# Kernel tuning notes

Measured on AMD Instinct MI355X. Metric: run time of the kernel, lower is better.

## Reference

```python
import jax, jax.numpy as jnp
import numpy as np

BS, P, D, C, ND, K, NC, H = 32, 196, 512, 100, 51, 50, 800, 8
LAMBDA, BETA, EPS = 0.5, 5.5, 1e-5


def _ln(x, g, b):
    m = x.mean(-1, keepdims=True)
    v = jnp.mean((x - m) ** 2, axis=-1, keepdims=True)
    return (x - m) / jnp.sqrt(v + EPS) * g + b


def _norm(x):
    return x / jnp.linalg.norm(x, axis=-1, keepdims=True)


def _bonder(x, kv, Wq, Wk, Wv, Wo, ln1_g, ln1_b, ln2_g, ln2_b, W1, b1, W2, b2):
    # cross-attn block: queries = text prompts [B,N,d], kv = retrieved patch feats [B,M,d]
    B, N, d = x.shape
    M = kv.shape[1]
    dh = d // H
    q = (_ln(x, ln1_g, ln1_b) @ Wq).reshape(B, N, H, dh)
    k = (kv @ Wk).reshape(B, M, H, dh)
    v = (kv @ Wv).reshape(B, M, H, dh)
    att = jax.nn.softmax(jnp.einsum('bnhd,bmhd->bhnm', q, k) / np.sqrt(dh).astype(np.float32), axis=-1)
    o = jnp.einsum('bhnm,bmhd->bnhd', att, v).reshape(B, N, d) @ Wo
    x = x + o
    h = _ln(x, ln2_g, ln2_b)
    return x + jax.nn.gelu(h @ W1 + b1) @ W2 + b2


def _dense_logits(gfeat, local, all_text, mean_text, topk):
    # gfeat [b,d], local [b,p,d], all_text [C,n,d], mean_text [C,d]
    base = gfeat @ mean_text.T                                   # [b,C]
    w = jnp.einsum('bd,bpd->bp', gfeat, local)                   # [b,p]
    atf = jnp.transpose(all_text, (1, 0, 2))                     # [n,C,d]
    v = jax.nn.softmax(jnp.einsum('cd,ncd->nc', mean_text, atf), axis=0)  # [n,C]
    sim = jnp.einsum('bpd,ncd->bcpn', local, atf)                # [b,C,p,n]
    vals, idx = jax.lax.top_k(jnp.transpose(sim, (0, 1, 3, 2)), topk)     # over patch dim
    sim_topk = jnp.transpose(vals, (0, 1, 3, 2))                 # [b,C,k,n]
    idx = jnp.transpose(idx, (0, 1, 3, 2))                       # [b,C,k,n]
    idx_w = idx[:, 0, :, 0]                                      # [b,k]
    w_topk = jax.nn.softmax(jnp.take_along_axis(w, idx_w, axis=1), axis=-1)  # [b,k]
    weight = jnp.einsum('bk,nc->bckn', w_topk, v)                # [b,C,k,n]
    return base + jnp.sum(sim_topk * weight, axis=(-2, -1))


def setup_inputs() -> dict:
    key = jax.random.key(0)
    ks = jax.random.split(key, 12)
    s = 0.02
    labels = jax.random.randint(ks[10], (BS,), 0, C)
    cache_labels = jax.random.randint(ks[11], (NC,), 0, C)
    return {
        'local_feat': jax.random.normal(ks[0], (BS, P, D)),
        'Wa': jnp.eye(D) + s * jax.random.normal(ks[1], (D, D)),
        'text_cache': jax.random.normal(ks[2], (C, ND, D)),
        'Wq': s * jax.random.normal(ks[3], (D, D)),
        'Wk': s * jax.random.normal(ks[4], (D, D)),
        'Wv': s * jax.random.normal(ks[5], (D, D)),
        'Wo': s * jax.random.normal(ks[6], (D, D)),
        'ln1_g': jnp.ones((D,)), 'ln1_b': jnp.zeros((D,)),
        'ln2_g': jnp.ones((D,)), 'ln2_b': jnp.zeros((D,)),
        'W1': s * jax.random.normal(ks[7], (D, 4 * D)), 'b1': jnp.zeros((4 * D,)),
        'W2': s * jax.random.normal(ks[8], (4 * D, D)), 'b2': jnp.zeros((D,)),
        'logit_scale': jnp.asarray(np.log(1.0 / 0.07), jnp.float32),
        'ensemble_scale': jnp.asarray(-2.0, jnp.float32),
        'raw_cache_local_feats': jax.random.normal(ks[9], (NC, P, D)),
        'cache_values': jax.nn.one_hot(cache_labels, C, dtype=jnp.float32),
        'labels': labels,
        'cache_labels': cache_labels,
    }


def reference(local_feat, Wa, text_cache, Wq, Wk, Wv, Wo, ln1_g, ln1_b, ln2_g, ln2_b,
              W1, b1, W2, b2, logit_scale, ensemble_scale, raw_cache_local_feats,
              cache_values, labels, cache_labels):
    bs = local_feat.shape[0]
    adapted_local = _norm(local_feat @ Wa.T)                      # [b,p,d]
    adapted_global = _norm(adapted_local.mean(axis=1))            # [b,d]
    base_text_mean = _norm(jax.lax.stop_gradient(text_cache).mean(axis=1))  # [C,d]
    sim_to_text = jax.lax.stop_gradient(adapted_local @ base_text_mean.T)   # [b,p,C]
    sim_target = sim_to_text[jnp.arange(bs), :, labels]           # [b,p]
    topk_idx = jax.lax.top_k(sim_target, K)[1]
    botk_idx = jax.lax.top_k(-sim_target, K)[1]
    topk_feats = jnp.take_along_axis(adapted_local, topk_idx[:, :, None], axis=1)  # [b,K,d]
    botk_feats = jnp.take_along_axis(adapted_local, botk_idx[:, :, None], axis=1)
    # training branch: bonder on ground-truth class prompts, scatter into bias_full
    l2p = text_cache[labels]                                      # [b,ND,d]
    text_bias = _bonder(l2p, jax.lax.stop_gradient(topk_feats),
                        Wq, Wk, Wv, Wo, ln1_g, ln1_b, ln2_g, ln2_b, W1, b1, W2, b2)
    bias_full = jnp.zeros((bs, C, ND, D), local_feat.dtype).at[jnp.arange(bs), labels].set(text_bias)
    bias_avg = bias_full.mean(axis=0)                             # [C,ND,d]
    refined = text_cache + LAMBDA * bias_avg
    refined_norm = _norm(refined)
    refined_mean_norm = _norm(refined_norm.mean(axis=1))
    ls = jnp.exp(logit_scale)
    inter = ls * _dense_logits(adapted_global, adapted_local, refined_norm, refined_mean_norm, K)
    # tip-adapter cache branch
    cache_adapted = _norm(raw_cache_local_feats @ Wa.T)           # [Nc,p,d]
    cache_sim = jax.lax.stop_gradient(cache_adapted @ base_text_mean.T)
    cache_sim_target = cache_sim[jnp.arange(cache_sim.shape[0]), :, cache_labels]
    cache_topk_idx = jax.lax.top_k(cache_sim_target, K)[1]
    cache_topk_feats = jnp.take_along_axis(cache_adapted, cache_topk_idx[:, :, None], axis=1)
    cache_keys = _norm(cache_topk_feats.mean(axis=1))             # [Nc,d]
    query_keys = _norm(topk_feats.mean(axis=1))                   # [b,d]
    affinity = jnp.exp(-BETA * (1.0 - query_keys @ cache_keys.T))
    intra = affinity @ cache_values                               # [b,C]
    scale = jax.nn.sigmoid(ensemble_scale)
    logits = inter * (1 - scale) + intra * ls * scale
    return (logits, inter, intra, adapted_global, topk_feats, botk_feats, refined_norm)
```

## Files before the change

kernel.cpp:

```cpp
#include <hip/hip_runtime.h>
#include <math.h>

#define DEV static __device__ __forceinline__

typedef __attribute__((ext_vector_type(8))) short short8v;
typedef __attribute__((ext_vector_type(8))) _Float16 half8v;
typedef __attribute__((ext_vector_type(4))) float f32x4;

DEV unsigned encf(float f){ unsigned b=__float_as_uint(f); return b ^ (0x80000000u | (unsigned)((int)b>>31)); }
DEV unsigned long long pkvi(float v, int idx){
  return ((unsigned long long)encf(v)<<32) | (unsigned long long)(0xffffffffu - (unsigned)idx);
}
DEV unsigned long long wave_max_ull(unsigned long long u){
  #pragma unroll
  for (int m=1;m<64;m<<=1){ unsigned long long o = __shfl_xor(u, m); if (o>u) u=o; }
  return u;
}
DEV float wave_sum(float v){
  #pragma unroll
  for (int m=32;m;m>>=1) v += __shfl_xor(v, m);
  return v;
}
DEV float blk_sum256(float v, float* scr){
  v = wave_sum(v);
  __syncthreads();
  if ((threadIdx.x & 63)==0) scr[threadIdx.x>>6] = v;
  __syncthreads();
  return scr[0]+scr[1]+scr[2]+scr[3];
}
DEV float gelu_f(float x){ return 0.5f*x*(1.f + tanhf(0.7978845608028654f*(x + 0.044715f*x*x*x))); }
DEV unsigned short f2bf(float x){
  unsigned u = __float_as_uint(x);
  unsigned r = (u + 0x7fffu + ((u>>16)&1u)) >> 16;
  return (unsigned short)r;
}
DEV float bf2f(unsigned short h){ return __uint_as_float(((unsigned)h)<<16); }
DEV void gld16(const void* g, void* l){
  __builtin_amdgcn_global_load_lds((const __attribute__((address_space(1))) unsigned int*)g,
                                   (__attribute__((address_space(3))) unsigned int*)l, 16, 0, 0);
}
template<int CTRL>
DEV float dppf(float x){
  return __int_as_float(__builtin_amdgcn_mov_dpp(__float_as_int(x), CTRL, 0xF, 0xF, false));
}

template<bool TRANSB, int EPI>
__global__ __launch_bounds__(256,2) void gemm128(
  const float* __restrict__ A, const float* __restrict__ B, float* __restrict__ Cp,
  const int M, const int N, const int K,
  const float* __restrict__ bias, const float* __restrict__ resid)
{
  __shared__ float As[16][132];
  __shared__ float Bs[16][132];
  const int t = threadIdx.x;
  const int row0 = blockIdx.x*128, col0 = blockIdx.y*128;
  const int tx = t & 15, ty = t >> 4;
  float acc[8][8];
  #pragma unroll
  for (int i=0;i<8;++i)
    #pragma unroll
    for (int j=0;j<8;++j) acc[i][j]=0.f;

  for (int k0=0; k0<K; k0+=16){
    #pragma unroll
    for (int it=0; it<2; ++it){
      int f = t + it*256;
      int m = f >> 2, kq = (f & 3) << 2;
      float4 v = make_float4(0.f,0.f,0.f,0.f);
      int gr = row0 + m;
      if (gr < M) v = *(const float4*)(A + (size_t)gr*K + (k0+kq));
      As[kq+0][m]=v.x; As[kq+1][m]=v.y; As[kq+2][m]=v.z; As[kq+3][m]=v.w;
    }
    if (TRANSB){
      #pragma unroll
      for (int it=0; it<2; ++it){
        int f = t + it*256;
        int n = f >> 2, kq = (f & 3) << 2;
        float4 v = make_float4(0.f,0.f,0.f,0.f);
        int gc = col0 + n;
        if (gc < N) v = *(const float4*)(B + (size_t)gc*K + (k0+kq));
        Bs[kq+0][n]=v.x; Bs[kq+1][n]=v.y; Bs[kq+2][n]=v.z; Bs[kq+3][n]=v.w;
      }
    } else {
      #pragma unroll
      for (int it=0; it<2; ++it){
        int f = t + it*256;
        int kk = f >> 5, n4 = (f & 31) << 2;
        float4 v = *(const float4*)(B + (size_t)(k0+kk)*N + (col0+n4));
        *(float4*)&Bs[kk][n4] = v;
      }
    }
    __syncthreads();
    #pragma unroll
    for (int k=0;k<16;++k){
      float a[8], bb[8];
      *(float4*)&a[0] = *(const float4*)&As[k][ty*4];
      *(float4*)&a[4] = *(const float4*)&As[k][64+ty*4];
      *(float4*)&bb[0] = *(const float4*)&Bs[k][tx*4];
      *(float4*)&bb[4] = *(const float4*)&Bs[k][64+tx*4];
      #pragma unroll
      for (int i=0;i<8;++i)
        #pragma unroll
        for (int j=0;j<8;++j) acc[i][j] = fmaf(a[i], bb[j], acc[i][j]);
    }
    __syncthreads();
  }

  #pragma unroll
  for (int i=0;i<8;++i){
    int gr = row0 + ((i<4)? (ty*4+i) : (64+ty*4+i-4));
    if (gr >= M) continue;
    #pragma unroll
    for (int jb=0;jb<2;++jb){
      int gc = col0 + (jb? (64+tx*4) : (tx*4));
      float4 vv;
      vv.x = acc[i][jb*4+0]; vv.y = acc[i][jb*4+1]; vv.z = acc[i][jb*4+2]; vv.w = acc[i][jb*4+3];
      if (EPI & 1){
        const float4 bv = *(const float4*)(bias + gc);
        vv.x += bv.x; vv.y += bv.y; vv.z += bv.z; vv.w += bv.w;
      }
      if (EPI & 2){
        vv.x = gelu_f(vv.x); vv.y = gelu_f(vv.y); vv.z = gelu_f(vv.z); vv.w = gelu_f(vv.w);
      }
      if (EPI & 4){
        const float4 rv = *(const float4*)(resid + (size_t)gr*N + gc);
        vv.x += rv.x; vv.y += rv.y; vv.z += rv.z; vv.w += rv.w;
      }
      *(float4*)(Cp + (size_t)gr*N + gc) = vv;
    }
  }
}

template<bool TRANS, bool SUBI>
__global__ __launch_bounds__(256) void k_convw(const float* __restrict__ W,
    unsigned short* __restrict__ hi, unsigned short* __restrict__ lo, int R, int C){
  int n = blockIdx.x;
  int K = TRANS ? R : C;
  for (int k = threadIdx.x; k < K; k += 256){
    float x = TRANS ? W[(size_t)k*C + n] : W[(size_t)n*C + k];
    if (SUBI && k==n) x -= 1.f;
    unsigned short h = f2bf(x);
    hi[(size_t)n*K + k] = h;
    if (lo) lo[(size_t)n*K + k] = f2bf(x - bf2f(h));
  }
}

__global__ __launch_bounds__(256) void k_convw4(
  const float* __restrict__ Wq, const float* __restrict__ Wk,
  const float* __restrict__ Wv, const float* __restrict__ Wo,
  unsigned short* __restrict__ qh, unsigned short* __restrict__ ql,
  unsigned short* __restrict__ kh, unsigned short* __restrict__ kl,
  unsigned short* __restrict__ vh, unsigned short* __restrict__ vl,
  unsigned short* __restrict__ oh, unsigned short* __restrict__ ol)
{
  int n = blockIdx.x;
  const float* W; unsigned short *hi, *lo;
  switch(blockIdx.y){
    case 0: W=Wq; hi=qh; lo=ql; break;
    case 1: W=Wk; hi=kh; lo=kl; break;
    case 2: W=Wv; hi=vh; lo=vl; break;
    default: W=Wo; hi=oh; lo=ol; break;
  }
  for (int k = threadIdx.x; k < 512; k += 256){
    float x = W[(size_t)k*512 + n];
    unsigned short h = f2bf(x);
    hi[(size_t)n*512 + k] = h;
    lo[(size_t)n*512 + k] = f2bf(x - bf2f(h));
  }
}

__global__ __launch_bounds__(256) void k_convd2(const float* __restrict__ Wa, unsigned short* __restrict__ Dfrag){
  int e = blockIdx.x;
  int tile = e>>4, lr = e&15;
  for (int d = threadIdx.x; d < 512; d += 256){
    float x = Wa[(size_t)e*512 + d] - (e==d ? 1.f : 0.f);
    union { _Float16 hh; unsigned short u; } cv;
    cv.hh = (_Float16)x;
    int ks = d>>5, q = (d>>3)&3, el = d&7;
    Dfrag[(size_t)(((tile*16+ks)*64 + q*16 + lr)*8 + el)] = cv.u;
  }
}

template<int EPI>
__global__ __launch_bounds__(256,2) void gemmAB(
  const unsigned short* __restrict__ Ahi, const unsigned short* __restrict__ Alo,
  const unsigned short* __restrict__ Bhi, const unsigned short* __restrict__ Blo,
  float* __restrict__ Cp, unsigned short* __restrict__ Chi, unsigned short* __restrict__ Clo,
  const int M, const int N, const int K,
  const float* __restrict__ bias, const float* __restrict__ resid)
{
  __shared__ __align__(16) char sm[32768];
  const int t = threadIdx.x, lane = t&63, wid = t>>6;
  const int row0 = blockIdx.x*128, col0 = blockIdx.y*128;
  f32x4 acc[2][8];
  #pragma unroll
  for (int i=0;i<2;++i)
    #pragma unroll
    for (int j=0;j<8;++j) acc[i][j] = (f32x4){0.f,0.f,0.f,0.f};

  int offA[2], offB[8];
  #pragma unroll
  for (int mt=0; mt<2; ++mt){
    int row = (2*wid+mt)*16 + (lane&15);
    int sp = (lane>>4) ^ ((row>>1)&3);
    offA[mt] = row*64 + sp*16;
  }
  #pragma unroll
  for (int nt=0; nt<8; ++nt){
    int row = nt*16 + (lane&15);
    int sp = (lane>>4) ^ ((row>>1)&3);
    offB[nt] = row*64 + sp*16;
  }

  const int nks = K >> 5;
  for (int ks=0; ks<nks; ++ks){
    #pragma unroll
    for (int i=0;i<2;++i){
      int s = i*256 + t, row = s>>2, sl2 = s&3, slog = sl2 ^ ((row>>1)&3);
      size_t ga = (size_t)(row0+row)*K + ks*32 + slog*8;
      size_t gb = (size_t)(col0+row)*K + ks*32 + slog*8;
      int dst = (i*256 + wid*64)*16;
      gld16(Ahi + ga, sm + dst);
      gld16(Alo + ga, sm + 8192 + dst);
      gld16(Bhi + gb, sm + 16384 + dst);
      gld16(Blo + gb, sm + 24576 + dst);
    }
    __syncthreads();
    short8v ah0 = *(short8v*)(sm + offA[0]);
    short8v ah1 = *(short8v*)(sm + offA[1]);
    short8v al0 = *(short8v*)(sm + 8192 + offA[0]);
    short8v al1 = *(short8v*)(sm + 8192 + offA[1]);
    #pragma unroll
    for (int nt=0; nt<8; ++nt){
      short8v bh = *(short8v*)(sm + 16384 + offB[nt]);
      short8v bl = *(short8v*)(sm + 24576 + offB[nt]);
      acc[0][nt] = __builtin_amdgcn_mfma_f32_16x16x32_bf16(ah0, bh, acc[0][nt], 0,0,0);
      acc[0][nt] = __builtin_amdgcn_mfma_f32_16x16x32_bf16(ah0, bl, acc[0][nt], 0,0,0);
      acc[0][nt] = __builtin_amdgcn_mfma_f32_16x16x32_bf16(al0, bh, acc[0][nt], 0,0,0);
      acc[1][nt] = __builtin_amdgcn_mfma_f32_16x16x32_bf16(ah1, bh, acc[1][nt], 0,0,0);
      acc[1][nt] = __builtin_amdgcn_mfma_f32_16x16x32_bf16(ah1, bl, acc[1][nt], 0,0,0);
      acc[1][nt] = __builtin_amdgcn_mfma_f32_16x16x32_bf16(al1, bh, acc[1][nt], 0,0,0);
    }
    __syncthreads();
  }

  #pragma unroll
  for (int mt=0; mt<2; ++mt){
    #pragma unroll
    for (int nt=0; nt<8; ++nt){
      int n = col0 + nt*16 + (lane&15);
      int mb = row0 + (2*wid+mt)*16 + (lane>>4)*4;
      #pragma unroll
      for (int j=0;j<4;++j){
        int m = mb + j;
        if (m < M){
          float v = acc[mt][nt][j];
          if (EPI & 1) v += bias[n];
          if (EPI & 2) v = gelu_f(v);
          if (EPI & 4) v += resid[(size_t)m*N + n];
          if (EPI & 8){
            unsigned short h = f2bf(v);
            Chi[(size_t)m*N + n] = h;
            Clo[(size_t)m*N + n] = f2bf(v - bf2f(h));
          } else {
            Cp[(size_t)m*N + n] = v;
          }
        }
      }
    }
  }
}

__global__ __launch_bounds__(256,2) void gemmABQKV(
  const unsigned short* __restrict__ lnH, const unsigned short* __restrict__ lnL,
  const unsigned short* __restrict__ tkH, const unsigned short* __restrict__ tkL,
  const unsigned short* __restrict__ qh, const unsigned short* __restrict__ ql,
  const unsigned short* __restrict__ kh, const unsigned short* __restrict__ kl,
  const unsigned short* __restrict__ vh, const unsigned short* __restrict__ vl,
  float* __restrict__ qb, float* __restrict__ kb, float* __restrict__ vbuf)
{
  __shared__ __align__(16) char sm[32768];
  const int z = blockIdx.z;
  const unsigned short* Ahi = (z==0)? lnH : tkH;
// ... 176 lines not shown
          float rh = (float)*(const _Float16*)(Alds + kse*8192 + row*64 + sll*16 + (o&7)*2);
          p = fmaf(U, 2.f*rh + U, p);
        }
        p += __shfl_xor(p,1); p += __shfl_xor(p,2); p += __shfl_xor(p,4); p += __shfl_xor(p,8);
        pacc[mt][j] += p;
      }
    }
  }

  __syncthreads();
  if ((lane&15)==0){
    #pragma unroll
    for (int mt=0; mt<4; ++mt)
      #pragma unroll
      for (int j=0;j<4;++j)
        n2x[wn][wm*64 + mt*16 + (lane>>4)*4 + j] = pacc[mt][j];
  }
  __syncthreads();
  if (t < 128)
    norm2[m0+t] = n2sq[t] + n2x[0][t] + n2x[1][t] + n2x[2][t] + n2x[3][t];
}

__global__ __launch_bounds__(256) void k_rownorm(const float* __restrict__ in, float* __restrict__ out,
                                                 unsigned short* __restrict__ bfo, int nrows){
  __shared__ float scr[4];
  int r = blockIdx.x, t = threadIdx.x; (void)nrows;
  const float* p = in + (size_t)r*512;
  float x0 = p[t], x1 = p[t+256];
  float ss = blk_sum256(x0*x0 + x1*x1, scr);
  float inv = 1.f/sqrtf(ss);
  float v0 = x0*inv, v1 = x1*inv;
  out[(size_t)r*512 + t] = v0;
  out[(size_t)r*512 + t + 256] = v1;
  if (bfo){
    size_t br = (size_t)(r/196)*256 + (r%196);
    bfo[br*512 + t]     = f2bf(v0);
    bfo[br*512 + t+256] = f2bf(v1);
  }
}

__global__ __launch_bounds__(256) void k_meanrows_norm(const float* __restrict__ in, int nper,
                                                       float* __restrict__ o1, float* __restrict__ o2){
  __shared__ float scr[4];
  int g = blockIdx.x, t = threadIdx.x;
  float s0=0.f, s1=0.f;
  const float* bp = in + (size_t)g*nper*512;
  for (int r=0;r<nper;++r){ s0 += bp[(size_t)r*512+t]; s1 += bp[(size_t)r*512+t+256]; }
  float ss = blk_sum256(s0*s0+s1*s1, scr);
  float inv = 1.f/sqrtf(ss);
  float v0 = s0*inv, v1 = s1*inv;
  o1[(size_t)g*512+t]=v0; o1[(size_t)g*512+t+256]=v1;
  if (o2){ o2[(size_t)g*512+t]=v0; o2[(size_t)g*512+t+256]=v1; }
}

__global__ __launch_bounds__(256) void k_zmat(const float* __restrict__ btm, const float* __restrict__ Wa, float* __restrict__ z){
  int c = blockIdx.x, t = threadIdx.x;
  float a0=0.f, a1=0.f;
  for (int d=0; d<512; ++d){
    float bv = btm[c*512+d];
    a0 = fmaf(bv, Wa[(size_t)d*512+t], a0);
    a1 = fmaf(bv, Wa[(size_t)d*512+t+256], a1);
  }
  z[c*512+t]=a0; z[c*512+t+256]=a1;
}

__global__ __launch_bounds__(256) void k_dot_bp(const float* __restrict__ AL, const float* __restrict__ vecs,
                                                const int* __restrict__ sel, float* __restrict__ outv, int mode){
  int wid = blockIdx.x*4 + (threadIdx.x>>6);
  int lane = threadIdx.x & 63;
  int b = wid/196;
  int vrow = sel ? sel[b] : (mode ? 0 : b);
  const float* a = AL + (size_t)wid*512 + lane*8;
  const float* v = vecs + (size_t)vrow*512 + lane*8;
  float4 a0 = *(const float4*)a, a1 = *(const float4*)(a+4);
  float4 v0 = *(const float4*)v, v1 = *(const float4*)(v+4);
  float s = a0.x*v0.x + a0.y*v0.y + a0.z*v0.z + a0.w*v0.w
          + a1.x*v1.x + a1.y*v1.y + a1.z*v1.z + a1.w*v1.w;
  s = wave_sum(s);
  if (lane==0) outv[wid] = s;
}

__global__ __launch_bounds__(256) void k_dot2(const float* __restrict__ AL, const float* __restrict__ AGw,
                                              const float* __restrict__ RN00,
                                              float* __restrict__ wbp, float* __restrict__ sLw){
  int wid = blockIdx.x*4 + (threadIdx.x>>6);
  int lane = threadIdx.x & 63;
  int b = wid/196;
  const float* a = AL + (size_t)wid*512 + lane*8;
  const float* v = AGw + (size_t)b*512 + lane*8;
  const float* w = RN00 + lane*8;
  float4 a0=*(const float4*)a, a1=*(const float4*)(a+4);
  float4 v0=*(const float4*)v, v1=*(const float4*)(v+4);
  float4 w0=*(const float4*)w, w1=*(const float4*)(w+4);
  float s1 = a0.x*v0.x+a0.y*v0.y+a0.z*v0.z+a0.w*v0.w + a1.x*v1.x+a1.y*v1.y+a1.z*v1.z+a1.w*v1.w;
  float s2 = a0.x*w0.x+a0.y*w0.y+a0.z*w0.z+a0.w*w0.w + a1.x*w1.x+a1.y*w1.y+a1.z*w1.z+a1.w*w1.w;
  s1 = wave_sum(s1); s2 = wave_sum(s2);
  if (lane==0){ wbp[wid] = s1; sLw[wid] = s2; }
}

__global__ __launch_bounds__(64) void k_topbot(const float* __restrict__ st, int* __restrict__ tki, int* __restrict__ bki){
  int b = blockIdx.x, lane = threadIdx.x;
  float v[4];
  #pragma unroll
  for (int s2=0;s2<4;++s2){ int p = lane + 64*s2; v[s2] = (p<196)? st[b*196+p] : -INFINITY; }
  for (int k=0;k<50;++k){
    unsigned long long best = pkvi(v[0], lane);
    { unsigned long long cc=pkvi(v[1],lane+64);  if(cc>best)best=cc; }
    { unsigned long long cc=pkvi(v[2],lane+128); if(cc>best)best=cc; }
    { unsigned long long cc=pkvi(v[3],lane+192); if(cc>best)best=cc; }
    best = wave_max_ull(best);
    int widx = (int)(0xffffffffu - (unsigned)(best & 0xffffffffu));
    if (lane==0) tki[b*50+k] = widx;
    if ((widx & 63)==lane) v[widx>>6] = -INFINITY;
  }
  #pragma unroll
  for (int s2=0;s2<4;++s2){ int p = lane + 64*s2; v[s2] = (p<196)? -st[b*196+p] : -INFINITY; }
  for (int k=0;k<50;++k){
    unsigned long long best = pkvi(v[0], lane);
    { unsigned long long cc=pkvi(v[1],lane+64);  if(cc>best)best=cc; }
    { unsigned long long cc=pkvi(v[2],lane+128); if(cc>best)best=cc; }
    { unsigned long long cc=pkvi(v[3],lane+192); if(cc>best)best=cc; }
    best = wave_max_ull(best);
    int widx = (int)(0xffffffffu - (unsigned)(best & 0xffffffffu));
    if (lane==0) bki[b*50+k] = widx;
    if ((widx & 63)==lane) v[widx>>6] = -INFINITY;
  }
}

__global__ __launch_bounds__(256) void k_gather_tb(const float* __restrict__ AL, const int* __restrict__ tki, const int* __restrict__ bki,
                                                   float* __restrict__ otk, float* __restrict__ obk, float* __restrict__ qk,
                                                   unsigned short* __restrict__ tkH, unsigned short* __restrict__ tkL){
  __shared__ float scr[4];
  int b = blockIdx.x, t = threadIdx.x;
  float a0=0.f, a1=0.f;
  for (int k=0;k<50;++k){
    int pt = tki[b*50+k];
    const float* rp = AL + ((size_t)b*196+pt)*512;
    float x0 = rp[t], x1 = rp[t+256];
    size_t ro = ((size_t)b*50+k)*512;
    otk[ro + t] = x0; otk[ro + t+256] = x1;
    unsigned short h0 = f2bf(x0), h1 = f2bf(x1);
    tkH[ro + t] = h0;      tkL[ro + t]     = f2bf(x0 - bf2f(h0));
    tkH[ro + t+256] = h1;  tkL[ro + t+256] = f2bf(x1 - bf2f(h1));
    a0 += x0; a1 += x1;
    int pb = bki[b*50+k];
    const float* rb = AL + ((size_t)b*196+pb)*512;
    obk[ro + t] = rb[t]; obk[ro + t+256] = rb[t+256];
  }
  float ss = blk_sum256(a0*a0+a1*a1, scr);
  float inv = 1.f/sqrtf(ss);
  qk[b*512+t] = a0*inv; qk[b*512+t+256] = a1*inv;
}

__global__ __launch_bounds__(256) void k_gather_x(const float* __restrict__ tc, const int* __restrict__ labels, float* __restrict__ xb){
  int r = blockIdx.x, t = threadIdx.x;
  int b = r/51, n = r%51;
  int lab = labels[b];
  const float* src = tc + ((size_t)lab*51 + n)*512;
  xb[(size_t)r*512+t] = src[t]; xb[(size_t)r*512+t+256] = src[t+256];
}

__global__ __launch_bounds__(256) void k_layernorm2(const float* __restrict__ in,
                                                    unsigned short* __restrict__ hi, unsigned short* __restrict__ lo,
                                                    const float* __restrict__ g, const float* __restrict__ be){
  __shared__ float scr[4];
  int r = blockIdx.x, t = threadIdx.x;
  const float* p = in + (size_t)r*512;
  float x0=p[t], x1=p[t+256];
  float s = blk_sum256(x0+x1, scr);
  float mean = s*(1.f/512.f);
  float ss = blk_sum256(x0*x0+x1*x1, scr);
  float var = ss*(1.f/512.f) - mean*mean;
  float inv = 1.f/sqrtf(var + 1e-5f);
  float v0 = (x0-mean)*inv*g[t]     + be[t];
  float v1 = (x1-mean)*inv*g[t+256] + be[t+256];
  unsigned short h0 = f2bf(v0), h1 = f2bf(v1);
  hi[(size_t)r*512+t]     = h0;  lo[(size_t)r*512+t]     = f2bf(v0 - bf2f(h0));
  hi[(size_t)r*512+t+256] = h1;  lo[(size_t)r*512+t+256] = f2bf(v1 - bf2f(h1));
}

__global__ __launch_bounds__(256) void k_attn2(const float* __restrict__ qb, const float* __restrict__ kb,
                                               const float* __restrict__ vb,
                                               unsigned short* __restrict__ obH, unsigned short* __restrict__ obL){
  int b = blockIdx.x, h = blockIdx.y, t = threadIdx.x;
  __shared__ float qh[51][65];
  __shared__ float kh[50][65];
  __shared__ float vh[50][65];
  __shared__ float S[51][52];
  for (int f=t; f<51*64; f+=256){ int n=f>>6, d=f&63; qh[n][d] = qb[((size_t)(b*51+n))*512 + h*64 + d]; }
  for (int f=t; f<50*64; f+=256){ int m=f>>6, d=f&63;
    kh[m][d] = kb[((size_t)(b*50+m))*512 + h*64 + d];
    vh[m][d] = vb[((size_t)(b*50+m))*512 + h*64 + d];
  }
  __syncthreads();
  for (int f=t; f<51*50; f+=256){
    int n=f/50, m=f%50;
    float s=0.f;
    #pragma unroll 8
    for (int d=0; d<64; ++d) s = fmaf(qh[n][d], kh[m][d], s);
    S[n][m] = s*0.125f;
  }
  __syncthreads();
  int w = t>>6, lane = t&63;
  for (int n=w; n<51; n+=4){
    float x = (lane<50)? S[n][lane] : -INFINITY;
    float mx = x;
    #pragma unroll
    for (int m2=32;m2;m2>>=1) mx = fmaxf(mx, __shfl_xor(mx,m2));
    float e = (lane<50)? expf(x-mx) : 0.f;
    float se = wave_sum(e);
    if (lane<50) S[n][lane] = e/se;
  }
  __syncthreads();
  for (int f=t; f<51*64; f+=256){
    int n=f>>6, d=f&63;
    float s=0.f;
    #pragma unroll 10
    for (int m=0;m<50;++m) s = fmaf(S[n][m], vh[m][d], s);
    size_t idx = ((size_t)(b*51+n))*512 + h*64 + d;
    unsigned short hh = f2bf(s);
    obH[idx] = hh; obL[idx] = f2bf(s - bf2f(hh));
  }
}

__global__ __launch_bounds__(256) void k_refined(const float* __restrict__ tc, const float* __restrict__ TB,
                                                 const int* __restrict__ labels, float* __restrict__ RN,
                                                 unsigned short* __restrict__ RNbf){
  __shared__ float scr[4];
  __shared__ int labL[32];
  int blk = blockIdx.x, t = threadIdx.x;
  int c = blk/51, n = blk%51;
  if (t<32) labL[t] = labels[t];
  __syncthreads();
  float r0=0.f, r1=0.f;
  for (int b=0;b<32;++b){
    if (labL[b]==c){
      const float* tb = TB + ((size_t)(b*51+n))*512;
      r0 += tb[t]; r1 += tb[t+256];
    }
  }
  const float* tcp = tc + ((size_t)(c*51+n))*512;
  r0 = tcp[t]     + r0*(1.f/64.f);
  r1 = tcp[t+256] + r1*(1.f/64.f);
  float ss = blk_sum256(r0*r0+r1*r1, scr);
  float inv = 1.f/sqrtf(ss);
  float v0 = r0*inv, v1 = r1*inv;
  RN[((size_t)(c*51+n))*512+t]     = v0;
  RN[((size_t)(c*51+n))*512+t+256] = v1;
  size_t br = (size_t)c*64 + n;
  RNbf[br*512 + t]     = f2bf(v0);
  RNbf[br*512 + t+256] = f2bf(v1);
}

__global__ __launch_bounds__(256) void k_vsm(const float* __restrict__ RN, const float* __restrict__ RMN, float* __restrict__ vsm){
  __shared__ float sv[51];
  int c = blockIdx.x, t = threadIdx.x, w = t>>6, lane = t&63;
  for (int n=w; n<51; n+=4){
    const float* a = RN + ((size_t)(c*51+n))*512 + lane*8;
    const float* m = RMN + (size_t)c*512 + lane*8;
    float4 a0=*(const float4*)a, a1=*(const float4*)(a+4);
    float4 m0=*(const float4*)m, m1=*(const float4*)(m+4);
    float s = a0.x*m0.x+a0.y*m0.y+a0.z*m0.z+a0.w*m0.w + a1.x*m1.x+a1.y*m1.y+a1.z*m1.z+a1.w*m1.w;
    s = wave_sum(s);
    if (lane==0) sv[n]=s;
  }
  __syncthreads();
  if (t<64){
    float x = (t<51)? sv[t] : -INFINITY;
    float mx = x;
    #pragma unroll
    for (int m2=32;m2;m2>>=1) mx = fmaxf(mx, __shfl_xor(mx,m2));
    float e = (t<51)? expf(x-mx) : 0.f;
    float se = wave_sum(e);
    if (t<51) vsm[c*51+t] = e/se;
  }
}

__global__ __launch_bounds__(64) void k_wtopk(const float* __restrict__ sLg,
                                              const float* __restrict__ wbp, float* __restrict__ wtk){
  __shared__ int idxL[50];
  int b = blockIdx.x, lane = threadIdx.x;
  float v[4];
  #pragma unroll
  for (int s2=0;s2<4;++s2){ int p = lane+64*s2; v[s2] = (p<196)? sLg[b*196+p] : -INFINITY; }
  for (int k=0;k<50;++k){
    unsigned long long best = pkvi(v[0], lane);
    { unsigned long long cc=pkvi(v[1],lane+64);  if(cc>best)best=cc; }
    { unsigned long long cc=pkvi(v[2],lane+128); if(cc>best)best=cc; }
    { unsigned long long cc=pkvi(v[3],lane+192); if(cc>best)best=cc; }
    best = wave_max_ull(best);
    int widx = (int)(0xffffffffu - (unsigned)(best & 0xffffffffu));
    if (lane==0) idxL[k]=widx;
    if ((widx&63)==lane) v[widx>>6] = -INFINITY;
  }
  __syncthreads();
  float wv = (lane<50)? wbp[b*196 + idxL[lane]] : -INFINITY;
  float mx = wv;
  #pragma unroll
  for (int m2=32;m2;m2>>=1) mx = fmaxf(mx, __shfl_xor(mx,m2));
  float e = (lane<50)? expf(wv-mx) : 0.f;
  float se = wave_sum(e);
  if (lane<50) wtk[b*50+lane] = e/se;
}

__global__ __launch_bounds__(256,3) void k_dense3(
  const unsigned short* __restrict__ ALbf, const unsigned short* __restrict__ RNbf,
  const float* __restrict__ RMN, const float* __restrict__ AG,
  const float* __restrict__ vsm, const float* __restrict__ wtk,
  const float* __restrict__ lsp, float* __restrict__ interw)
{
  __shared__ __align__(16) char smem[52224];
  __shared__ float red[8];
// ... 175 lines not shown
      v[s2] = (p<196)? cdot[(size_t)i*196+p] * (1.f/sqrtf(norm2[(size_t)i*196+p])) : -INFINITY;
    }
    for (int k=0;k<50;++k){
      unsigned long long best = pkvi(v[0], lane);
      { unsigned long long cc=pkvi(v[1],lane+64);  if(cc>best)best=cc; }
      { unsigned long long cc=pkvi(v[2],lane+128); if(cc>best)best=cc; }
      { unsigned long long cc=pkvi(v[3],lane+192); if(cc>best)best=cc; }
      best = wave_max_ull(best);
      int widx = (int)(0xffffffffu - (unsigned)(best & 0xffffffffu));
      if (lane==0){ idxL[k]=widx; invL[k] = 1.f/sqrtf(norm2[(size_t)i*196+widx]); }
      if ((widx&63)==lane) v[widx>>6] = -INFINITY;
    }
  }
  __syncthreads();
  float a0=0.f, a1=0.f;
  #pragma unroll
  for (int kc=0; kc<5; ++kc){
    float x0[10], x1[10];
    #pragma unroll
    for (int j=0;j<10;++j){
      const float* rp = raw + ((size_t)i*196 + idxL[kc*10+j])*512;
      x0[j] = rp[t]; x1[j] = rp[t+256];
    }
    #pragma unroll
    for (int j=0;j<10;++j){
      float iv = invL[kc*10+j];
      a0 = fmaf(x0[j], iv, a0);
      a1 = fmaf(x1[j], iv, a1);
    }
  }
  unsigned short h0 = f2bf(a0), h1 = f2bf(a1);
  rbH[(size_t)i*512+t]     = h0;  rbL[(size_t)i*512+t]     = f2bf(a0 - bf2f(h0));
  rbH[(size_t)i*512+t+256] = h1;  rbL[(size_t)i*512+t+256] = f2bf(a1 - bf2f(h1));
}

__global__ __launch_bounds__(256) void k_aff(const float* __restrict__ qk, const float* __restrict__ ck, float* __restrict__ aff){
  int gid = blockIdx.x*4 + (threadIdx.x>>6);
  int lane = threadIdx.x&63;
  int b = gid/800, i = gid%800;
  const float* a = qk + (size_t)b*512 + lane*8;
  const float* v = ck + (size_t)i*512 + lane*8;
  float4 a0=*(const float4*)a, a1=*(const float4*)(a+4);
  float4 v0=*(const float4*)v, v1=*(const float4*)(v+4);
  float s = a0.x*v0.x+a0.y*v0.y+a0.z*v0.z+a0.w*v0.w + a1.x*v1.x+a1.y*v1.y+a1.z*v1.z+a1.w*v1.w;
  s = wave_sum(s);
  if (lane==0) aff[gid] = expf(-5.5f*(1.f - s));
}

__global__ __launch_bounds__(128) void k_intra(const float* __restrict__ aff, const float* __restrict__ cv, float* __restrict__ intra){
  __shared__ float affL[800];
  int b = blockIdx.x, t = threadIdx.x;
  for (int f=t; f<800; f+=128) affL[f] = aff[b*800+f];
  __syncthreads();
  if (t<100){
    float s=0.f;
    for (int i=0;i<800;++i) s = fmaf(affL[i], cv[(size_t)i*100+t], s);
    intra[b*100+t]=s;
  }
}

__global__ void k_final(const float* __restrict__ interw, const float* __restrict__ intraw,
                        const float* __restrict__ lsp, const float* __restrict__ esp, float* __restrict__ outp){
  int idx = blockIdx.x*256 + threadIdx.x;
  if (idx < 3200){
    float ls = expf(lsp[0]);
    float sc = 1.f/(1.f + expf(-esp[0]));
    float iv = interw[idx], ia = intraw[idx];
    outp[idx]        = iv*(1.f-sc) + ia*ls*sc;
    outp[3200+idx]   = iv;
    outp[6400+idx]   = ia;
  }
}

extern "C" void kernel_launch(void* const* d_in, const int* in_sizes, int n_in,
                              void* d_out, int out_size, void* d_ws, size_t ws_size,
                              hipStream_t stream)
{
  (void)in_sizes; (void)n_in; (void)out_size; (void)ws_size;
  const float* lf   = (const float*)d_in[0];
  const float* Wa   = (const float*)d_in[1];
  const float* tc   = (const float*)d_in[2];
  const float* Wq   = (const float*)d_in[3];
  const float* Wk   = (const float*)d_in[4];
  const float* Wv   = (const float*)d_in[5];
  const float* Wo   = (const float*)d_in[6];
  const float* ln1g = (const float*)d_in[7];
  const float* ln1b = (const float*)d_in[8];
  const float* ln2g = (const float*)d_in[9];
  const float* ln2b = (const float*)d_in[10];
  const float* W1   = (const float*)d_in[11];
  const float* b1   = (const float*)d_in[12];
  const float* W2   = (const float*)d_in[13];
  const float* b2   = (const float*)d_in[14];
  const float* lsp  = (const float*)d_in[15];
  const float* esp  = (const float*)d_in[16];
  const float* raw  = (const float*)d_in[17];
  const float* cv   = (const float*)d_in[18];
  const int* labels = (const int*)d_in[19];
  const int* clab   = (const int*)d_in[20];

  float* out = (float*)d_out;
  float* outAG = out + 9600;
  float* outTK = out + 25984;
  float* outBK = out + 845184;
  float* outRN = out + 1664384;

  float* wsf = (float*)d_ws;
  size_t o = 0;
  #define WALLOC(name, n) float* name = wsf + o; o += (size_t)(n);
  WALLOC(AL,    6272*512)
  WALLOC(xb,    1632*512)
  WALLOC(qb,    1632*512)
  WALLOC(kb,    1600*512)
  WALLOC(vbuf,  1600*512)
  WALLOC(x2,    1632*512)
  WALLOC(TB,    1632*512)
  WALLOC(btm,   100*512)
  WALLOC(zm,    100*512)
  WALLOC(RMN,   100*512)
  WALLOC(vsm,   5100)
  WALLOC(st,    6272)
  WALLOC(wbp,   6272)
  WALLOC(sLw,   6272)
  WALLOC(AGw,   32*512)
  WALLOC(qkb,   32*512)
  WALLOC(wtk,   1600)
  WALLOC(norm2, 156800)
  WALLOC(cdot,  156800)
  WALLOC(mbuf,  800*512)
  WALLOC(ckb,   800*512)
  WALLOC(aff,   25600)
  WALLOC(interw,3200)
  WALLOC(intraw,3200)
  #undef WALLOC
  int* tki = (int*)(wsf + o); o += 1600;
  int* bki = (int*)(wsf + o); o += 1600;
  unsigned short* ALbf = (unsigned short*)(wsf + o); o += (size_t)32*256*512/2;
  unsigned short* RNbf = (unsigned short*)(wsf + o); o += (size_t)100*64*512/2;
  #define WALLOC16(name, n) unsigned short* name = (unsigned short*)(wsf + o); o += ((size_t)(n)+1)/2;
  WALLOC16(waHi, 262144)  WALLOC16(waLo, 262144)
  WALLOC16(wqHi, 262144)  WALLOC16(wqLo, 262144)
  WALLOC16(wkHi, 262144)  WALLOC16(wkLo, 262144)
  WALLOC16(wvHi, 262144)  WALLOC16(wvLo, 262144)
  WALLOC16(woHi, 262144)  WALLOC16(woLo, 262144)
  WALLOC16(w1Hi, 1048576) WALLOC16(w1Lo, 1048576)
  WALLOC16(w2Hi, 1048576) WALLOC16(w2Lo, 1048576)
  WALLOC16(dfrag, 262144)
  WALLOC16(ln1H, 851968)  WALLOC16(ln1L, 851968)
  WALLOC16(h2H,  851968)  WALLOC16(h2L,  851968)
  WALLOC16(obH,  851968)  WALLOC16(obL,  851968)
  WALLOC16(tkH,  851968)  WALLOC16(tkL,  851968)
  WALLOC16(y1H,  3407872) WALLOC16(y1L,  3407872)
  WALLOC16(rbH,  458752)  WALLOC16(rbL,  458752)
  #undef WALLOC16

  k_convw<false,false><<<dim3(512), dim3(256), 0, stream>>>(Wa, waHi, waLo, 512,512);
  k_convw4<<<dim3(512,4), dim3(256), 0, stream>>>(Wq,Wk,Wv,Wo, wqHi,wqLo, wkHi,wkLo, wvHi,wvLo, woHi,woLo);
  k_convw<true ,false><<<dim3(2048), dim3(256), 0, stream>>>(W1, w1Hi, w1Lo, 512,2048);
  k_convw<true ,false><<<dim3(512), dim3(256), 0, stream>>>(W2, w2Hi, w2Lo, 2048,512);
  k_convd2<<<dim3(512), dim3(256), 0, stream>>>(Wa, dfrag);

  hipMemsetAsync(ALbf, 0, ((size_t)32*256*512 + (size_t)100*64*512)*2, stream);

  gemm128<true,0><<<dim3(49,4), dim3(256), 0, stream>>>(lf, Wa, AL, 6272,512,512, nullptr,nullptr);
  k_rownorm<<<dim3(6272), dim3(256), 0, stream>>>(AL, AL, ALbf, 6272);
  k_meanrows_norm<<<dim3(32), dim3(256), 0, stream>>>(AL, 196, AGw, outAG);
  k_meanrows_norm<<<dim3(100), dim3(256), 0, stream>>>(tc, 51, btm, (float*)nullptr);
  k_zmat<<<dim3(100), dim3(256), 0, stream>>>(btm, Wa, zm);
  k_dot_bp<<<dim3(1568), dim3(256), 0, stream>>>(AL, btm, labels, st, 0);
  k_topbot<<<dim3(32), dim3(64), 0, stream>>>(st, tki, bki);
  k_gather_tb<<<dim3(32), dim3(256), 0, stream>>>(AL, tki, bki, outTK, outBK, qkb, tkH, tkL);
  k_gather_x<<<dim3(1632), dim3(256), 0, stream>>>(tc, labels, xb);
  k_layernorm2<<<dim3(1632), dim3(256), 0, stream>>>(xb, ln1H, ln1L, ln1g, ln1b);
  gemmABQKV<<<dim3(13,4,3), dim3(256), 0, stream>>>(ln1H,ln1L, tkH,tkL, wqHi,wqLo, wkHi,wkLo, wvHi,wvLo, qb, kb, vbuf);
  k_attn2<<<dim3(32,8), dim3(256), 0, stream>>>(qb, kb, vbuf, obH, obL);
  gemmAB<4><<<dim3(13,4), dim3(256), 0, stream>>>(obH, obL, woHi, woLo, x2, nullptr, nullptr, 1632,512,512, nullptr, xb);
  k_layernorm2<<<dim3(1632), dim3(256), 0, stream>>>(x2, h2H, h2L, ln2g, ln2b);
  gemmAB<11><<<dim3(13,16), dim3(256), 0, stream>>>(h2H, h2L, w1Hi, w1Lo, nullptr, y1H, y1L, 1632,2048,512, b1, nullptr);
  gemmAB<5><<<dim3(13,4), dim3(256), 0, stream>>>(y1H, y1L, w2Hi, w2Lo, TB, nullptr, nullptr, 1632,512,2048, b2, x2);
  k_refined<<<dim3(5100), dim3(256), 0, stream>>>(tc, TB, labels, outRN, RNbf);
  k_meanrows_norm<<<dim3(100), dim3(256), 0, stream>>>(outRN, 51, RMN, (float*)nullptr);
  k_vsm<<<dim3(100), dim3(256), 0, stream>>>(outRN, RMN, vsm);
  k_dot2<<<dim3(1568), dim3(256), 0, stream>>>(AL, AGw, outRN, wbp, sLw);
  k_wtopk<<<dim3(32), dim3(64), 0, stream>>>(sLw, wbp, wtk);
  k_dense3<<<dim3(100,32), dim3(256), 0, stream>>>(ALbf, RNbf, RMN, AGw, vsm, wtk, lsp, interw);
  k_un7<<<dim3(1225), dim3(512), 0, stream>>>(raw, dfrag, zm, clab, cdot, norm2);
  k_cache_sel<<<dim3(800), dim3(256), 0, stream>>>(cdot, norm2, raw, rbH, rbL);
  gemmAB<0><<<dim3(7,4), dim3(256), 0, stream>>>(rbH, rbL, waHi, waLo, mbuf, nullptr, nullptr, 800,512,512, nullptr, nullptr);
  k_rownorm<<<dim3(800), dim3(256), 0, stream>>>(mbuf, ckb, (unsigned short*)nullptr, 800);
  k_aff<<<dim3(6400), dim3(256), 0, stream>>>(qkb, ckb, aff);
  k_intra<<<dim3(32), dim3(128), 0, stream>>>(aff, cv, intraw);
  k_final<<<dim3(13), dim3(256), 0, stream>>>(interw, intraw, lsp, esp, out);
}
```

Measured before the change: 1.060 ms.

## Run local-feature projection on split-bf16 MFMA GEMM and fuse gather with LayerNorm

The fp32 SIMT gemm128 that projected local features through Wa is removed. The local features are now converted to hi/lo bf16 pairs and the projection goes through the existing split-precision matrix-core gemmAB path. Separately, the text-row gather and the first LayerNorm are fused into one kernel, which saves a launch and a global round trip. The price is an extra conversion pass over the 6272x512 input and extra workspace, and split-bf16 accuracy replaces exact fp32 in that GEMM.

```diff
diff --git a/kernel.cpp b/kernel.cpp
--- a/kernel.cpp
+++ b/kernel.cpp
@@ -42,93 +42,6 @@
 template<int CTRL>
 DEV float dppf(float x){
   return __int_as_float(__builtin_amdgcn_mov_dpp(__float_as_int(x), CTRL, 0xF, 0xF, false));
-}
-
-template<bool TRANSB, int EPI>
-__global__ __launch_bounds__(256,2) void gemm128(
-  const float* __restrict__ A, const float* __restrict__ B, float* __restrict__ Cp,
-  const int M, const int N, const int K,
-  const float* __restrict__ bias, const float* __restrict__ resid)
-{
-  __shared__ float As[16][132];
-  __shared__ float Bs[16][132];
-  const int t = threadIdx.x;
-  const int row0 = blockIdx.x*128, col0 = blockIdx.y*128;
-  const int tx = t & 15, ty = t >> 4;
-  float acc[8][8];
-  #pragma unroll
-  for (int i=0;i<8;++i)
-    #pragma unroll
-    for (int j=0;j<8;++j) acc[i][j]=0.f;
-
-  for (int k0=0; k0<K; k0+=16){
-    #pragma unroll
-    for (int it=0; it<2; ++it){
-      int f = t + it*256;
-      int m = f >> 2, kq = (f & 3) << 2;
-      float4 v = make_float4(0.f,0.f,0.f,0.f);
-      int gr = row0 + m;
-      if (gr < M) v = *(const float4*)(A + (size_t)gr*K + (k0+kq));
-      As[kq+0][m]=v.x; As[kq+1][m]=v.y; As[kq+2][m]=v.z; As[kq+3][m]=v.w;
-    }
-    if (TRANSB){
-      #pragma unroll
-      for (int it=0; it<2; ++it){
-        int f = t + it*256;
-        int n = f >> 2, kq = (f & 3) << 2;
-        float4 v = make_float4(0.f,0.f,0.f,0.f);
-        int gc = col0 + n;
-        if (gc < N) v = *(const float4*)(B + (size_t)gc*K + (k0+kq));
-        Bs[kq+0][n]=v.x; Bs[kq+1][n]=v.y; Bs[kq+2][n]=v.z; Bs[kq+3][n]=v.w;
-      }
-    } else {
-      #pragma unroll
-      for (int it=0; it<2; ++it){
-        int f = t + it*256;
-        int kk = f >> 5, n4 = (f & 31) << 2;
-        float4 v = *(const float4*)(B + (size_t)(k0+kk)*N + (col0+n4));
-        *(float4*)&Bs[kk][n4] = v;
-      }
-    }
-    __syncthreads();
-    #pragma unroll
-    for (int k=0;k<16;++k){
-      float a[8], bb[8];
-      *(float4*)&a[0] = *(const float4*)&As[k][ty*4];
-      *(float4*)&a[4] = *(const float4*)&As[k][64+ty*4];
-      *(float4*)&bb[0] = *(const float4*)&Bs[k][tx*4];
-      *(float4*)&bb[4] = *(const float4*)&Bs[k][64+tx*4];
-      #pragma unroll
-      for (int i=0;i<8;++i)
-        #pragma unroll
-        for (int j=0;j<8;++j) acc[i][j] = fmaf(a[i], bb[j], acc[i][j]);
-    }
-    __syncthreads();
-  }
-
-  #pragma unroll
-  for (int i=0;i<8;++i){
-    int gr = row0 + ((i<4)? (ty*4+i) : (64+ty*4+i-4));
-    if (gr >= M) continue;
-    #pragma unroll
-    for (int jb=0;jb<2;++jb){
-      int gc = col0 + (jb? (64+tx*4) : (tx*4));
-      float4 vv;
-      vv.x = acc[i][jb*4+0]; vv.y = acc[i][jb*4+1]; vv.z = acc[i][jb*4+2]; vv.w = acc[i][jb*4+3];
-      if (EPI & 1){
-        const float4 bv = *(const float4*)(bias + gc);
-        vv.x += bv.x; vv.y += bv.y; vv.z += bv.z; vv.w += bv.w;
-      }
-      if (EPI & 2){
-        vv.x = gelu_f(vv.x); vv.y = gelu_f(vv.y); vv.z = gelu_f(vv.z); vv.w = gelu_f(vv.w);
-      }
-      if (EPI & 4){
-        const float4 rv = *(const float4*)(resid + (size_t)gr*N + gc);
-        vv.x += rv.x; vv.y += rv.y; vv.z += rv.z; vv.w += rv.w;
-      }
-      *(float4*)(Cp + (size_t)gr*N + gc) = vv;
-    }
-  }
 }
 
 template<bool TRANS, bool SUBI>
@@ -611,12 +524,27 @@
   qk[b*512+t] = a0*inv; qk[b*512+t+256] = a1*inv;
 }
 
-__global__ __launch_bounds__(256) void k_gather_x(const float* __restrict__ tc, const int* __restrict__ labels, float* __restrict__ xb){
+__global__ __launch_bounds__(256) void k_gxln(const float* __restrict__ tc, const int* __restrict__ labels,
+                                              const float* __restrict__ g, const float* __restrict__ be,
+                                              float* __restrict__ xb,
+                                              unsigned short* __restrict__ hi, unsigned short* __restrict__ lo){
+  __shared__ float scr[4];
   int r = blockIdx.x, t = threadIdx.x;
   int b = r/51, n = r%51;
   int lab = labels[b];
   const float* src = tc + ((size_t)lab*51 + n)*512;
-  xb[(size_t)r*512+t] = src[t]; xb[(size_t)r*512+t+256] = src[t+256];
+  float x0 = src[t], x1 = src[t+256];
+  xb[(size_t)r*512+t] = x0; xb[(size_t)r*512+t+256] = x1;
+  float s = blk_sum256(x0+x1, scr);
+  float mean = s*(1.f/512.f);
+  float ss = blk_sum256(x0*x0+x1*x1, scr);
+  float var = ss*(1.f/512.f) - mean*mean;
+  float inv = 1.f/sqrtf(var + 1e-5f);
+  float v0 = (x0-mean)*inv*g[t]     + be[t];
+  float v1 = (x1-mean)*inv*g[t+256] + be[t+256];
+  unsigned short h0 = f2bf(v0), h1 = f2bf(v1);
+  hi[(size_t)r*512+t]     = h0;  lo[(size_t)r*512+t]     = f2bf(v0 - bf2f(h0));
+  hi[(size_t)r*512+t+256] = h1;  lo[(size_t)r*512+t+256] = f2bf(v1 - bf2f(h1));
 }
 
 __global__ __launch_bounds__(256) void k_layernorm2(const float* __restrict__ in,
@@ -1098,6 +1026,7 @@
   WALLOC16(tkH,  851968)  WALLOC16(tkL,  851968)
   WALLOC16(y1H,  3407872) WALLOC16(y1L,  3407872)
   WALLOC16(rbH,  458752)  WALLOC16(rbL,  458752)
+  WALLOC16(lfH,  3211264) WALLOC16(lfL,  3211264)
   #undef WALLOC16
 
   k_convw<false,false><<<dim3(512), dim3(256), 0, stream>>>(Wa, waHi, waLo, 512,512);
@@ -1105,10 +1034,11 @@
   k_convw<true ,false><<<dim3(2048), dim3(256), 0, stream>>>(W1, w1Hi, w1Lo, 512,2048);
   k_convw<true ,false><<<dim3(512), dim3(256), 0, stream>>>(W2, w2Hi, w2Lo, 2048,512);
   k_convd2<<<dim3(512), dim3(256), 0, stream>>>(Wa, dfrag);
+  k_convw<false,false><<<dim3(6272), dim3(256), 0, stream>>>(lf, lfH, lfL, 6272,512);
 
   hipMemsetAsync(ALbf, 0, ((size_t)32*256*512 + (size_t)100*64*512)*2, stream);
 
-  gemm128<true,0><<<dim3(49,4), dim3(256), 0, stream>>>(lf, Wa, AL, 6272,512,512, nullptr,nullptr);
+  gemmAB<0><<<dim3(49,4), dim3(256), 0, stream>>>(lfH, lfL, waHi, waLo, AL, nullptr, nullptr, 6272,512,512, nullptr, nullptr);
   k_rownorm<<<dim3(6272), dim3(256), 0, stream>>>(AL, AL, ALbf, 6272);
   k_meanrows_norm<<<dim3(32), dim3(256), 0, stream>>>(AL, 196, AGw, outAG);
   k_meanrows_norm<<<dim3(100), dim3(256), 0, stream>>>(tc, 51, btm, (float*)nullptr);
@@ -1116,8 +1046,7 @@
   k_dot_bp<<<dim3(1568), dim3(256), 0, stream>>>(AL, btm, labels, st, 0);
   k_topbot<<<dim3(32), dim3(64), 0, stream>>>(st, tki, bki);
   k_gather_tb<<<dim3(32), dim3(256), 0, stream>>>(AL, tki, bki, outTK, outBK, qkb, tkH, tkL);
-  k_gather_x<<<dim3(1632), dim3(256), 0, stream>>>(tc, labels, xb);
-  k_layernorm2<<<dim3(1632), dim3(256), 0, stream>>>(xb, ln1H, ln1L, ln1g, ln1b);
+  k_gxln<<<dim3(1632), dim3(256), 0, stream>>>(tc, labels, ln1g, ln1b, xb, ln1H, ln1L);
   gemmABQKV<<<dim3(13,4,3), dim3(256), 0, stream>>>(ln1H,ln1L, tkH,tkL, wqHi,wqLo, wkHi,wkLo, wvHi,wvLo, qb, kb, vbuf);
   k_attn2<<<dim3(32,8), dim3(256), 0, stream>>>(qb, kb, vbuf, obH, obL);
   gemmAB<4><<<dim3(13,4), dim3(256), 0, stream>>>(obH, obL, woHi, woLo, x2, nullptr, nullptr, 1632,512,512, nullptr, xb);
```

New measurement: 1.013 ms. -4.5%, faster.
